# Performance work log

Hardware: AMD Instinct MI355X
Metric: run time of the kernel (lower is better)

Reference implementation:

```python
import jax, jax.numpy as jnp
import numpy as np

N, K, D = 16384, 32, 256
NEG_SLOPE = 0.01  # torch F.leaky_relu default


def setup_inputs() -> dict:
    key = jax.random.key(0)
    k1, k2, k3, k4 = jax.random.split(key, 4)
    scale = 1.0 / np.sqrt(D)
    return {
        "target": jax.random.normal(k1, (N, D), dtype=jnp.float32),
        "middle": jax.random.normal(k2, (N, K, D), dtype=jnp.float32),
        "W": jax.random.normal(k3, (D, D), dtype=jnp.float32) * scale,
        "b": jnp.zeros((D,), dtype=jnp.float32),
        "a_w": jax.random.normal(k4, (1, D), dtype=jnp.float32) * scale,
        "a_b": jnp.zeros((1,), dtype=jnp.float32),
    }


def reference(target, middle, W, b, a_w, a_b):
    # attention_weight applied to both target and middle (bias added to each,
    # matching the torch code which sums two Linear outputs)
    pt = target @ W.T + b              # [N, D]
    pm = middle @ W.T + b              # [N, K, D]
    h = pt[:, None, :] + pm            # [N, K, D]
    # a_weight: D -> 1
    score = h @ a_w.T + a_b            # [N, K, 1]
    score = jax.nn.leaky_relu(score, negative_slope=NEG_SLOPE)
    coef = jax.nn.softmax(score, axis=-2)   # softmax over neighbor dim K
    neighbor_feature = jnp.sum(coef * middle, axis=-2)  # [N, D]
    return neighbor_feature
```

## Files before the change

### kernel.cpp

```cpp
#include <hip/hip_runtime.h>

#define N_ 16384
#define K_ 32
#define D_ 256
#define NEG_SLOPE 0.01f

__global__ __launch_bounds__(1024) void prep_kernel(
    const float* __restrict__ W, const float* __restrict__ b,
    const float* __restrict__ a_w, const float* __restrict__ a_b,
    float* __restrict__ ws) {
  __shared__ float part[4][D_];
  const int t = threadIdx.x;
  const int dd = t >> 8;
  const int e = t & 255;
  float acc = 0.f;
#pragma unroll 8
  for (int j = 0; j < 64; ++j) {
    const int d = dd * 64 + j;
    acc += a_w[d] * W[d * D_ + e];
  }
  part[dd][e] = acc;
  __syncthreads();
  if (t < D_) ws[t] = part[0][t] + part[1][t] + part[2][t] + part[3][t];
  __syncthreads();
  if (t < D_) part[0][t] = b[t] * a_w[t];
  __syncthreads();
  if (t == 0) {
    float s = 0.f;
    for (int i = 0; i < D_; ++i) s += part[0][i];
    ws[D_] = 2.f * s + a_b[0];
  }
}

__global__ __launch_bounds__(256) void attn_agg_kernel(
    const float* __restrict__ target, const float* __restrict__ middle,
    const float* __restrict__ ws, float* __restrict__ out) {
  __shared__ __align__(16) float part[4][D_];
  __shared__ float sdot[K_];
  __shared__ float scoef[K_];
  __shared__ float stp[4];

  const int t = threadIdx.x;
  const int kg = t >> 6;
  const int l = t & 63;
  const int n = blockIdx.x;

  const float4* m4p = (const float4*)(middle + (size_t)n * K_ * D_);
  float4 m[8];
#pragma unroll
  for (int j = 0; j < 8; ++j) m[j] = m4p[(kg * 8 + j) * 64 + l];

  const float4 vv = ((const float4*)ws)[l];
  const float vt = ws[t];
  const float cadd = ws[D_];
  const float tg = target[(size_t)n * D_ + t];

  float pd[8];
#pragma unroll
  for (int j = 0; j < 8; ++j)
    pd[j] = m[j].x * vv.x + m[j].y * vv.y + m[j].z * vv.z + m[j].w * vv.w;

#pragma unroll
  for (int j = 0; j < 8; ++j) pd[j] += __shfl_xor(pd[j], 32);
  float q0 = (l & 32) ? pd[4] : pd[0];
  float q1 = (l & 32) ? pd[5] : pd[1];
  float q2 = (l & 32) ? pd[6] : pd[2];
  float q3 = (l & 32) ? pd[7] : pd[3];
  q0 += __shfl_xor(q0, 16);
  q1 += __shfl_xor(q1, 16);
  q2 += __shfl_xor(q2, 16);
  q3 += __shfl_xor(q3, 16);
  float r0 = (l & 16) ? q2 : q0;
  float r1 = (l & 16) ? q3 : q1;
  r0 += __shfl_xor(r0, 8);
  r1 += __shfl_xor(r1, 8);
  float s = (l & 8) ? r1 : r0;
  s += __shfl_xor(s, 4);
  s += __shfl_xor(s, 2);
  s += __shfl_xor(s, 1);
  if ((l & 7) == 0) {
    const int j_own = ((l >> 5) & 1) * 4 + ((l >> 4) & 1) * 2 + ((l >> 3) & 1);
    sdot[kg * 8 + j_own] = s;
  }

  float tp = tg * vt;
#pragma unroll
  for (int off = 1; off < 64; off <<= 1) tp += __shfl_xor(tp, off);
  if (l == 0) stp[kg] = tp;
  __syncthreads();

  if (t < 64) {
    const float tdot = stp[0] + stp[1] + stp[2] + stp[3];
    const int k = t & 31;
    float sc = sdot[k] + tdot + cadd;
    sc = sc > 0.f ? sc : NEG_SLOPE * sc;
    float mx = sc;
    mx = fmaxf(mx, __shfl_xor(mx, 1));
    mx = fmaxf(mx, __shfl_xor(mx, 2));
    mx = fmaxf(mx, __shfl_xor(mx, 4));
    mx = fmaxf(mx, __shfl_xor(mx, 8));
    mx = fmaxf(mx, __shfl_xor(mx, 16));
    float ex = __expf(sc - mx);
    float sum = ex;
    sum += __shfl_xor(sum, 1);
    sum += __shfl_xor(sum, 2);
    sum += __shfl_xor(sum, 4);
    sum += __shfl_xor(sum, 8);
    sum += __shfl_xor(sum, 16);
    if (t < 32) scoef[k] = ex / sum;
  }
  __syncthreads();

  float4 acc = make_float4(0.f, 0.f, 0.f, 0.f);
#pragma unroll
  for (int j = 0; j < 8; ++j) {
    const float cf = scoef[kg * 8 + j];
    acc.x += cf * m[j].x;
    acc.y += cf * m[j].y;
    acc.z += cf * m[j].z;
    acc.w += cf * m[j].w;
  }
  *(float4*)(&part[kg][4 * l]) = acc;
  __syncthreads();

  out[(size_t)n * D_ + t] = part[0][t] + part[1][t] + part[2][t] + part[3][t];
}

extern "C" void kernel_launch(void* const* d_in, const int* in_sizes, int n_in,
                              void* d_out, int out_size, void* d_ws, size_t ws_size,
                              hipStream_t stream) {
  const float* target = (const float*)d_in[0];
  const float* middle = (const float*)d_in[1];
  const float* W      = (const float*)d_in[2];
  const float* b      = (const float*)d_in[3];
  const float* a_w    = (const float*)d_in[4];
  const float* a_b    = (const float*)d_in[5];
  float* out = (float*)d_out;
  float* ws  = (float*)d_ws;

  prep_kernel<<<1, 1024, 0, stream>>>(W, b, a_w, a_b, ws);
  attn_agg_kernel<<<N_, 256, 0, stream>>>(target, middle, ws, out);
}
```

Baseline: 113.7 us.

## Split prep reduction across blocks with atomics and widen aggregation blocks to 512 threads

The one-block prep kernel becomes 32 blocks. Each block reduces 8 rows of W against a_w and atomically adds into a workspace that a memset now zeroes first, so the serial single-block reduction is shortened. The main kernel moves to 512 threads per block, with each wave holding 4 neighbor rows instead of 8. This halves per-thread register use and adds waves in flight to hide memory latency. In exchange there is an extra memset launch, atomic accumulation whose summation order varies between runs, and a cross-wave reduction over 8 partial sums instead of 4.

```diff
diff --git a/kernel.cpp b/kernel.cpp
--- a/kernel.cpp
+++ b/kernel.cpp
@@ -5,37 +5,36 @@
 #define D_ 256
 #define NEG_SLOPE 0.01f
 
-__global__ __launch_bounds__(1024) void prep_kernel(
+__global__ __launch_bounds__(256) void prep_kernel(
     const float* __restrict__ W, const float* __restrict__ b,
     const float* __restrict__ a_w, const float* __restrict__ a_b,
     float* __restrict__ ws) {
-  __shared__ float part[4][D_];
   const int t = threadIdx.x;
-  const int dd = t >> 8;
-  const int e = t & 255;
+  const int i = blockIdx.x;
   float acc = 0.f;
-#pragma unroll 8
-  for (int j = 0; j < 64; ++j) {
-    const int d = dd * 64 + j;
-    acc += a_w[d] * W[d * D_ + e];
+#pragma unroll
+  for (int j = 0; j < 8; ++j) {
+    const int d = i * 8 + j;
+    acc += a_w[d] * W[d * D_ + t];
   }
-  part[dd][e] = acc;
-  __syncthreads();
-  if (t < D_) ws[t] = part[0][t] + part[1][t] + part[2][t] + part[3][t];
-  __syncthreads();
-  if (t < D_) part[0][t] = b[t] * a_w[t];
-  __syncthreads();
-  if (t == 0) {
-    float s = 0.f;
-    for (int i = 0; i < D_; ++i) s += part[0][i];
-    ws[D_] = 2.f * s + a_b[0];
+  atomicAdd(&ws[t], acc);
+
+  if (i == 0) {
+    float s = b[t] * a_w[t];
+#pragma unroll
+    for (int off = 1; off < 64; off <<= 1) s += __shfl_xor(s, off);
+    __shared__ float sp[4];
+    if ((t & 63) == 0) sp[t >> 6] = s;
+    __syncthreads();
+    if (t == 0)
+      atomicAdd(&ws[D_], 2.f * (sp[0] + sp[1] + sp[2] + sp[3]) + a_b[0]);
   }
 }
 
-__global__ __launch_bounds__(256) void attn_agg_kernel(
+__global__ __launch_bounds__(512, 8) void attn_agg_kernel(
     const float* __restrict__ target, const float* __restrict__ middle,
     const float* __restrict__ ws, float* __restrict__ out) {
-  __shared__ __align__(16) float part[4][D_];
+  __shared__ __align__(16) float part[8][D_];
   __shared__ float sdot[K_];
   __shared__ float scoef[K_];
   __shared__ float stp[4];
@@ -46,47 +45,38 @@
   const int n = blockIdx.x;
 
   const float4* m4p = (const float4*)(middle + (size_t)n * K_ * D_);
-  float4 m[8];
+  float4 m[4];
 #pragma unroll
-  for (int j = 0; j < 8; ++j) m[j] = m4p[(kg * 8 + j) * 64 + l];
+  for (int j = 0; j < 4; ++j) m[j] = m4p[(kg * 4 + j) * 64 + l];
 
   const float4 vv = ((const float4*)ws)[l];
-  const float vt = ws[t];
   const float cadd = ws[D_];
-  const float tg = target[(size_t)n * D_ + t];
 
-  float pd[8];
+  float pd[4];
 #pragma unroll
-  for (int j = 0; j < 8; ++j)
+  for (int j = 0; j < 4; ++j)
     pd[j] = m[j].x * vv.x + m[j].y * vv.y + m[j].z * vv.z + m[j].w * vv.w;
 
 #pragma unroll
-  for (int j = 0; j < 8; ++j) pd[j] += __shfl_xor(pd[j], 32);
-  float q0 = (l & 32) ? pd[4] : pd[0];
-  float q1 = (l & 32) ? pd[5] : pd[1];
-  float q2 = (l & 32) ? pd[6] : pd[2];
-  float q3 = (l & 32) ? pd[7] : pd[3];
+  for (int j = 0; j < 4; ++j) pd[j] += __shfl_xor(pd[j], 32);
+  float q0 = (l & 32) ? pd[2] : pd[0];
+  float q1 = (l & 32) ? pd[3] : pd[1];
   q0 += __shfl_xor(q0, 16);
   q1 += __shfl_xor(q1, 16);
-  q2 += __shfl_xor(q2, 16);
-  q3 += __shfl_xor(q3, 16);
-  float r0 = (l & 16) ? q2 : q0;
-  float r1 = (l & 16) ? q3 : q1;
-  r0 += __shfl_xor(r0, 8);
-  r1 += __shfl_xor(r1, 8);
-  float s = (l & 8) ? r1 : r0;
-  s += __shfl_xor(s, 4);
-  s += __shfl_xor(s, 2);
-  s += __shfl_xor(s, 1);
-  if ((l & 7) == 0) {
-    const int j_own = ((l >> 5) & 1) * 4 + ((l >> 4) & 1) * 2 + ((l >> 3) & 1);
-    sdot[kg * 8 + j_own] = s;
+  float r = (l & 16) ? q1 : q0;
+  r += __shfl_xor(r, 8);
+  r += __shfl_xor(r, 4);
+  r += __shfl_xor(r, 2);
+  r += __shfl_xor(r, 1);
+  if ((l & 15) == 0)
+    sdot[kg * 4 + ((l >> 5) * 2 + ((l >> 4) & 1))] = r;
+
+  if (t < D_) {
+    float tp = target[(size_t)n * D_ + t] * ws[t];
+#pragma unroll
+    for (int off = 1; off < 64; off <<= 1) tp += __shfl_xor(tp, off);
+    if (l == 0) stp[kg] = tp;
   }
-
-  float tp = tg * vt;
-#pragma unroll
-  for (int off = 1; off < 64; off <<= 1) tp += __shfl_xor(tp, off);
-  if (l == 0) stp[kg] = tp;
   __syncthreads();
 
   if (t < 64) {
@@ -113,8 +103,8 @@
 
   float4 acc = make_float4(0.f, 0.f, 0.f, 0.f);
 #pragma unroll
-  for (int j = 0; j < 8; ++j) {
-    const float cf = scoef[kg * 8 + j];
+  for (int j = 0; j < 4; ++j) {
+    const float cf = scoef[kg * 4 + j];
     acc.x += cf * m[j].x;
     acc.y += cf * m[j].y;
     acc.z += cf * m[j].z;
@@ -123,7 +113,12 @@
   *(float4*)(&part[kg][4 * l]) = acc;
   __syncthreads();
 
-  out[(size_t)n * D_ + t] = part[0][t] + part[1][t] + part[2][t] + part[3][t];
+  if (t < D_) {
+    float o = 0.f;
+#pragma unroll
+    for (int w = 0; w < 8; ++w) o += part[w][t];
+    out[(size_t)n * D_ + t] = o;
+  }
 }
 
 extern "C" void kernel_launch(void* const* d_in, const int* in_sizes, int n_in,
@@ -138,6 +133,7 @@
   float* out = (float*)d_out;
   float* ws  = (float*)d_ws;
 
-  prep_kernel<<<1, 1024, 0, stream>>>(W, b, a_w, a_b, ws);
-  attn_agg_kernel<<<N_, 256, 0, stream>>>(target, middle, ws, out);
+  hipMemsetAsync(ws, 0, (D_ + 1) * sizeof(float), stream);
+  prep_kernel<<<32, 256, 0, stream>>>(W, b, a_w, a_b, ws);
+  attn_agg_kernel<<<N_, 512, 0, stream>>>(target, middle, ws, out);
 }
```

Result: faster. 110.8 us (-2.5%).
